# Performance work log

Hardware: AMD Instinct MI355X
Metric: run time of the kernel (lower is better)

Reference implementation:

```python
import jax, jax.numpy as jnp
import numpy as np


def setup_inputs() -> dict:
    key = jax.random.key(0)
    k1, k2 = jax.random.split(key)
    E, D, N = 1250000, 64, 50000
    values = jax.random.normal(k1, (E, D), dtype=jnp.float32)
    segment_ids = jnp.sort(jax.random.randint(k2, (E,), 0, N, dtype=jnp.int64))
    return {"values": values, "segment_ids": segment_ids, "num_segments": N}


def reference(values, segment_ids, num_segments):
    # Segmented mean: equivalent to torch.cat([n.mean(0, keepdim=True) for n in neighbor])
    # over the packed ragged representation. Single fused pass instead of per-segment kernels.
    seg_sum = jax.ops.segment_sum(values, segment_ids, num_segments=num_segments,
                                  indices_are_sorted=True)  # [N, D]
    counts = jax.ops.segment_sum(jnp.ones((values.shape[0],), dtype=values.dtype),
                                 segment_ids, num_segments=num_segments,
                                 indices_are_sorted=True)  # [N]
    # guard against empty segments (original torch would produce NaN / error there)
    return seg_sum / jnp.maximum(counts, 1.0)[:, None]
```

## Files before the change

kernel.cpp:

```cpp
#include <hip/hip_runtime.h>


#define SPW 8
#define WPB 4

typedef float f4 __attribute__((ext_vector_type(4)));

__global__ __launch_bounds__(256) void seg_bounds_kernel(
    const int* __restrict__ seg_ids,
    int*       __restrict__ offs,
    int E, int N)
{
    const int q    = blockIdx.x * blockDim.x + threadIdx.x;
    const int base = q << 2;
    if (base >= E) return;

    int id0, id1, id2, id3;
    int nv = E - base;
    if (nv >= 4) {
        const int4 v = *reinterpret_cast<const int4*>(seg_ids + base);
        id0 = v.x; id1 = v.y; id2 = v.z; id3 = v.w;
    } else {
        id0 = seg_ids[base];
        id1 = (nv > 1) ? seg_ids[base + 1] : id0;
        id2 = (nv > 2) ? seg_ids[base + 2] : id1;
        id3 = id2;
    }

    int prev = (base > 0) ? seg_ids[base - 1] : -1;

    for (int s = prev + 1; s <= id0; ++s) offs[s] = base + 0;
    if (nv > 1) for (int s = id0 + 1; s <= id1; ++s) offs[s] = base + 1;
    if (nv > 2) for (int s = id1 + 1; s <= id2; ++s) offs[s] = base + 2;
    if (nv > 3) for (int s = id2 + 1; s <= id3; ++s) offs[s] = base + 3;

    if (base + 4 >= E) {
        for (int s = id3 + 1; s <= N; ++s) offs[s] = E;
    }
}

__global__ __launch_bounds__(256) void seg_mean_kernel(
    const float* __restrict__ values,
    const int*   __restrict__ offs,
    float*       __restrict__ out,
    int N)
{
    const int wave = threadIdx.x >> 6;
    const int wid  = blockIdx.x * WPB + wave;
    const int sg0  = wid * SPW;
    if (sg0 >= N) return;

    const int t = threadIdx.x & 63;

    int myoff = 0;
    if (t <= SPW) myoff = offs[min(sg0 + t, N)];

    const int rsub = t >> 4;
    const int c4   = (t & 15) << 2;

    const int nseg = min(SPW, N - sg0);
    for (int k = 0; k < nseg; ++k) {
        const int s     = sg0 + k;
        const int start = __shfl(myoff, k, 64);
        const int end   = __shfl(myoff, k + 1, 64);
        const int count = end - start;

        const f4* p = reinterpret_cast<const f4*>(
            values + (size_t)start * 64 + (t << 2));

        f4 a0 = {0.f, 0.f, 0.f, 0.f};
        f4 a1 = {0.f, 0.f, 0.f, 0.f};

        int r = start + rsub;
        for (; r + 4 < end; r += 8, p += 128) {
            const f4 v0 = __builtin_nontemporal_load(p);
            const f4 v1 = __builtin_nontemporal_load(p + 64);
            a0 += v0;
            a1 += v1;
        }
        if (r < end) {
            a0 += __builtin_nontemporal_load(p);
        }
        a0 += a1;

        a0.x += __shfl_xor(a0.x, 16, 64);
        a0.y += __shfl_xor(a0.y, 16, 64);
        a0.z += __shfl_xor(a0.z, 16, 64);
        a0.w += __shfl_xor(a0.w, 16, 64);
        a0.x += __shfl_xor(a0.x, 32, 64);
        a0.y += __shfl_xor(a0.y, 32, 64);
        a0.z += __shfl_xor(a0.z, 32, 64);
        a0.w += __shfl_xor(a0.w, 32, 64);

        if (t < 16) {
            const float inv = (count > 0) ? (1.0f / (float)count) : 0.0f;
            f4 o = a0 * inv;
            *reinterpret_cast<f4*>(out + (size_t)s * 64 + c4) = o;
        }
    }
}

extern "C" void kernel_launch(void* const* d_in, const int* in_sizes, int n_in,
                              void* d_out, int out_size, void* d_ws, size_t ws_size,
                              hipStream_t stream) {
    const float* values  = (const float*)d_in[0];
    const int*   seg_ids = (const int*)d_in[1];
    float*       out     = (float*)d_out;
    int*         offs    = (int*)d_ws;

    const int E = in_sizes[1];
    const int N = out_size / 64;

    const int quads  = (E + 3) / 4;
    const int nwaves = (N + SPW - 1) / SPW;
    const int nblk   = (nwaves + WPB - 1) / WPB;

    seg_bounds_kernel<<<dim3((quads + 255) / 256), dim3(256), 0, stream>>>(seg_ids, offs, E, N);
    seg_mean_kernel<<<dim3(nblk), dim3(256), 0, stream>>>(values, offs, out, N);
}
```

Baseline: 70.99 us.

## Process two segments per wave in a single merged streaming loop

Each wave now handles two adjacent segments instead of eight. It streams their combined row range in one loop and routes each row into one of two accumulators by comparing against the boundary. The aim is more waves in flight for memory-level parallelism and no per-segment loop overhead or serialization within a wave. Nontemporal loads are replaced by ordinary loads, and the per-row branch adds some ALU work.

Result: no change. 70.85 us (-0.2%).

```diff
diff --git a/kernel.cpp b/kernel.cpp
--- a/kernel.cpp
+++ b/kernel.cpp
@@ -1,7 +1,6 @@
 #include <hip/hip_runtime.h>
 
 
-#define SPW 8
 #define WPB 4
 
 typedef float f4 __attribute__((ext_vector_type(4)));
@@ -39,6 +38,13 @@
     }
 }
 
+__device__ __forceinline__ void fold(f4& a) {
+    a.x += __shfl_xor(a.x, 16, 64); a.y += __shfl_xor(a.y, 16, 64);
+    a.z += __shfl_xor(a.z, 16, 64); a.w += __shfl_xor(a.w, 16, 64);
+    a.x += __shfl_xor(a.x, 32, 64); a.y += __shfl_xor(a.y, 32, 64);
+    a.z += __shfl_xor(a.z, 32, 64); a.w += __shfl_xor(a.w, 32, 64);
+}
+
 __global__ __launch_bounds__(256) void seg_mean_kernel(
     const float* __restrict__ values,
     const int*   __restrict__ offs,
@@ -47,55 +53,50 @@
 {
     const int wave = threadIdx.x >> 6;
     const int wid  = blockIdx.x * WPB + wave;
-    const int sg0  = wid * SPW;
-    if (sg0 >= N) return;
+    const int s0   = wid * 2;
+    if (s0 >= N) return;
 
-    const int t = threadIdx.x & 63;
+    const int t   = threadIdx.x & 63;
+    const bool two = (s0 + 1) < N;
 
-    int myoff = 0;
-    if (t <= SPW) myoff = offs[min(sg0 + t, N)];
+    const int b0 = offs[s0];
+    const int b1 = offs[s0 + 1];
+    const int b2 = two ? offs[s0 + 2] : b1;
 
     const int rsub = t >> 4;
     const int c4   = (t & 15) << 2;
 
-    const int nseg = min(SPW, N - sg0);
-    for (int k = 0; k < nseg; ++k) {
-        const int s     = sg0 + k;
-        const int start = __shfl(myoff, k, 64);
-        const int end   = __shfl(myoff, k + 1, 64);
-        const int count = end - start;
+    const f4* p = reinterpret_cast<const f4*>(
+        values + (size_t)b0 * 64 + (t << 2));
 
-        const f4* p = reinterpret_cast<const f4*>(
-            values + (size_t)start * 64 + (t << 2));
+    f4 x0 = {0.f,0.f,0.f,0.f}, x1 = {0.f,0.f,0.f,0.f};
+    f4 y0 = {0.f,0.f,0.f,0.f}, y1 = {0.f,0.f,0.f,0.f};
 
-        f4 a0 = {0.f, 0.f, 0.f, 0.f};
-        f4 a1 = {0.f, 0.f, 0.f, 0.f};
+    int r = b0 + rsub;
+    for (; r + 4 < b2; r += 8, p += 128) {
+        const f4 v0 = p[0];
+        const f4 v1 = p[64];
+        if (r < b1)     x0 += v0; else y0 += v0;
+        if (r + 4 < b1) x1 += v1; else y1 += v1;
+    }
+    if (r < b2) {
+        const f4 v0 = p[0];
+        if (r < b1) x0 += v0; else y0 += v0;
+    }
+    x0 += x1;
+    y0 += y1;
 
-        int r = start + rsub;
-        for (; r + 4 < end; r += 8, p += 128) {
-            const f4 v0 = __builtin_nontemporal_load(p);
-            const f4 v1 = __builtin_nontemporal_load(p + 64);
-            a0 += v0;
-            a1 += v1;
-        }
-        if (r < end) {
-            a0 += __builtin_nontemporal_load(p);
-        }
-        a0 += a1;
+    fold(x0);
+    fold(y0);
 
-        a0.x += __shfl_xor(a0.x, 16, 64);
-        a0.y += __shfl_xor(a0.y, 16, 64);
-        a0.z += __shfl_xor(a0.z, 16, 64);
-        a0.w += __shfl_xor(a0.w, 16, 64);
-        a0.x += __shfl_xor(a0.x, 32, 64);
-        a0.y += __shfl_xor(a0.y, 32, 64);
-        a0.z += __shfl_xor(a0.z, 32, 64);
-        a0.w += __shfl_xor(a0.w, 32, 64);
-
-        if (t < 16) {
-            const float inv = (count > 0) ? (1.0f / (float)count) : 0.0f;
-            f4 o = a0 * inv;
-            *reinterpret_cast<f4*>(out + (size_t)s * 64 + c4) = o;
+    if (t < 16) {
+        const int   c0   = b1 - b0;
+        const float inv0 = (c0 > 0) ? (1.0f / (float)c0) : 0.0f;
+        *reinterpret_cast<f4*>(out + (size_t)s0 * 64 + c4) = x0 * inv0;
+        if (two) {
+            const int   c1   = b2 - b1;
+            const float inv1 = (c1 > 0) ? (1.0f / (float)c1) : 0.0f;
+            *reinterpret_cast<f4*>(out + (size_t)(s0 + 1) * 64 + c4) = y0 * inv1;
         }
     }
 }
@@ -112,7 +113,7 @@
     const int N = out_size / 64;
 
     const int quads  = (E + 3) / 4;
-    const int nwaves = (N + SPW - 1) / SPW;
+    const int nwaves = (N + 1) / 2;
     const int nblk   = (nwaves + WPB - 1) / WPB;
 
     seg_bounds_kernel<<<dim3((quads + 255) / 256), dim3(256), 0, stream>>>(seg_ids, offs, E, N);
```
